# Kernel optimization log

Measured on AMD Instinct MI355X. Metric: run time of the kernel, lower is better.

Reference implementation:

```python
import jax, jax.numpy as jnp
import numpy as np
from math import ceil

SCALE = (0.25, 0.25)
IM_SIZE = (1080, 1920)
KERNEL_WIDTH = 4.0


def _cubic(x):
    absx = np.abs(x)
    absx2 = absx * absx
    absx3 = absx2 * absx
    return ((1.5 * absx3 - 2.5 * absx2 + 1) * (absx <= 1)
            + (-0.5 * absx3 + 2.5 * absx2 - 4 * absx + 2) * ((1 < absx) * (absx <= 2)))


def _contributions(in_length, out_length, scale):
    # MATLAB-style imresize contributions (matches the torch module's numpy code)
    if scale < 1:
        h = lambda v: scale * _cubic(scale * v)
        kernel_width = KERNEL_WIDTH / scale
    else:
        h = _cubic
        kernel_width = KERNEL_WIDTH
    x = np.arange(1, out_length + 1).astype(np.float64)
    u = x / scale + 0.5 * (1 - 1 / scale)
    left = np.floor(u - kernel_width / 2)
    P = int(ceil(kernel_width)) + 2
    ind = np.expand_dims(left, axis=1) + np.arange(P) - 1
    indices = ind.astype(np.int32)
    weights = h(np.expand_dims(u, axis=1) - indices - 1)
    weights = weights / np.sum(weights, axis=1, keepdims=True)
    aux = np.concatenate((np.arange(in_length), np.arange(in_length - 1, -1, -1))).astype(np.int32)
    indices = aux[np.mod(indices, aux.size)]
    keep = np.nonzero(np.any(weights, axis=0))[0]
    return weights[:, keep].astype(np.float32), indices[:, keep].astype(np.int64)


def setup_inputs() -> dict:
    key = jax.random.key(0)
    B, C = 8, 3
    H, W = IM_SIZE
    x = jax.random.normal(key, (B, C, H, W), dtype=jnp.float32)
    out_h = int(ceil(SCALE[0] * H))
    out_w = int(ceil(SCALE[1] * W))
    w_h, idx_h = _contributions(H, out_h, SCALE[0])
    w_w, idx_w = _contributions(W, out_w, SCALE[1])
    return {
        "x": x,
        "w_h": jnp.asarray(w_h), "idx_h": jnp.asarray(idx_h),
        "w_w": jnp.asarray(w_w), "idx_w": jnp.asarray(idx_w),
    }


def reference(x, w_h, idx_h, w_w, idx_w):
    # x: [B, C, H, W] -> work in [B, H, W, C] like the torch transpose dance
    xb = jnp.transpose(x, (0, 2, 3, 1))
    # scale is equal along both axes -> argsort order is [0, 1]: resize H then W
    # gather rows: [B, outH, P, W, C], contract over P with weights [outH, P]
    g = xb[:, idx_h, :, :]
    xb = jnp.einsum("op,bopwc->bowc", w_h, g)
    # gather cols: [B, outH, outW, P, C]
    g = xb[:, :, idx_w, :]
    xb = jnp.einsum("op,bhopc->bhoc", w_w, g)
    return jnp.transpose(xb, (0, 3, 1, 2))
```

## Files before the change

kernel.cpp:

```cpp
#include <hip/hip_runtime.h>

namespace {

constexpr int H  = 1080;
constexpr int W  = 1920;
constexpr int OH = 270;
constexpr int OW = 480;
constexpr int KT = 16;
constexpr int G  = 7;
constexpr int NCHUNK = 38;
constexpr int COLS = 1024;
constexpr int VSTRIDE = 1028;

__global__ __launch_bounds__(256) void bicubic_tile(
    const float* __restrict__ x,
    const float* __restrict__ wh,
    const float* __restrict__ ww,
    float*       __restrict__ out)
{
    __shared__ float vbuf[G * VSTRIDE];

    const int tid  = threadIdx.x;
    const int tile = blockIdx.x;
    const int oh0  = 2 + G * blockIdx.y;
    const int bc   = blockIdx.z;

    const int ow_base = (tile == 0) ? 2   : 255;
    const int Nw      = (tile == 0) ? 253 : 223;
    const int c0      = 4 * ow_base - 6;
    const int r0      = 4 * oh0 - 6;

    float wr[KT];
    __builtin_memcpy(wr, wh + (size_t)oh0 * KT, sizeof(wr));

    int c = c0 + 4 * tid;
    if (c > W - 4) c = W - 4;
    const float* __restrict__ col = x + ((size_t)bc * H + (size_t)r0) * W + c;

    float acc[4][4];
    #pragma unroll
    for (int m = 0; m < 4; ++m)
        #pragma unroll
        for (int cc = 0; cc < 4; ++cc) acc[m][cc] = 0.0f;

    for (int q = 0; q < G + 3; ++q) {
        #pragma unroll
        for (int p = 0; p < 4; ++p) {
            float v[4];
            __builtin_memcpy(v, col + (size_t)(4 * q + p) * W, 16);
            #pragma unroll
            for (int cc = 0; cc < 4; ++cc) {
                acc[0][cc] = fmaf(wr[p],      v[cc], acc[0][cc]);
                acc[1][cc] = fmaf(wr[4 + p],  v[cc], acc[1][cc]);
                acc[2][cc] = fmaf(wr[8 + p],  v[cc], acc[2][cc]);
                acc[3][cc] = fmaf(wr[12 + p], v[cc], acc[3][cc]);
            }
        }
        if (q >= 3) {
            __builtin_memcpy(&vbuf[(q - 3) * VSTRIDE + 4 * tid], acc[3], 16);
        }
        #pragma unroll
        for (int cc = 0; cc < 4; ++cc) {
            acc[3][cc] = acc[2][cc];
            acc[2][cc] = acc[1][cc];
            acc[1][cc] = acc[0][cc];
            acc[0][cc] = 0.0f;
        }
    }
    __syncthreads();

    if (tid < Nw) {
        const int ow = ow_base + tid;
        float wt[KT];
        __builtin_memcpy(wt, ww + (size_t)ow * KT, sizeof(wt));
        float* __restrict__ obase =
            out + ((size_t)bc * OH + oh0) * OW + ow;
        #pragma unroll
        for (int t = 0; t < G; ++t) {
            float v[KT];
            __builtin_memcpy(v, &vbuf[t * VSTRIDE + 4 * tid], sizeof(v));
            float s0 = 0.f, s1 = 0.f;
            #pragma unroll
            for (int k = 0; k < KT; k += 2) {
                s0 = fmaf(v[k],     wt[k],     s0);
                s1 = fmaf(v[k + 1], wt[k + 1], s1);
            }
            obase[(size_t)t * OW] = s0 + s1;
        }
    }
}

constexpr int EDGE_FULL = 4 * OW;
constexpr int EDGE_TOT  = EDGE_FULL + (OH - 4) * 4;

__global__ __launch_bounds__(256) void bicubic_edge(
    const float* __restrict__ x,
    const float* __restrict__ wh,
    const int*   __restrict__ ih,
    const float* __restrict__ ww,
    const int*   __restrict__ iw,
    float*       __restrict__ out)
{
    const int idx = blockIdx.x * blockDim.x + threadIdx.x;
    const int bc  = blockIdx.y;
    if (idx >= EDGE_TOT) return;

    int oh, ow;
    if (idx < EDGE_FULL) {
        int e = idx / OW;
        ow = idx - e * OW;
        oh = (e < 2) ? e : OH - 4 + e;
    } else {
        int t = idx - EDGE_FULL;
        int e = t & 3;
        oh = 2 + (t >> 2);
        ow = (e < 2) ? e : OW - 4 + e;
    }

    const float* __restrict__ img = x + (size_t)bc * ((size_t)H * W);

    float wt[KT];
    __builtin_memcpy(wt, ww + (size_t)ow * KT, sizeof(wt));
    int ir[KT];
    __builtin_memcpy(ir, iw + (size_t)ow * KT, sizeof(ir));

    bool fast = true;
    #pragma unroll
    for (int k = 1; k < KT; ++k) fast = fast && (ir[k] == ir[0] + k);
    const int i0 = ir[0];

    float acc = 0.0f;
    #pragma unroll 4
    for (int kh = 0; kh < KT; ++kh) {
        const int   r = ih[oh * KT + kh];
        const float w = wh[oh * KT + kh];
        const float* row = img + (size_t)r * W;
        float h = 0.0f;
        if (fast) {
            float v[KT];
            __builtin_memcpy(v, row + i0, sizeof(v));
            #pragma unroll
            for (int k = 0; k < KT; ++k) h = fmaf(v[k], wt[k], h);
        } else {
            #pragma unroll
            for (int k = 0; k < KT; ++k) h = fmaf(row[ir[k]], wt[k], h);
        }
        acc = fmaf(w, h, acc);
    }
    out[((size_t)bc * OH + oh) * OW + ow] = acc;
}

__global__ __launch_bounds__(256) void bicubic_generic(
    const float* __restrict__ x,
    const float* __restrict__ wh,
    const int*   __restrict__ ih,
    const float* __restrict__ ww,
    const int*   __restrict__ iw,
    float*       __restrict__ out,
    int Kh, int Kw, int total)
{
    int t = blockIdx.x * blockDim.x + threadIdx.x;
    if (t >= total) return;
    int ow = t % OW;
    int oh = (t / OW) % OH;
    int bc = t / (OW * OH);
    const float* img = x + (size_t)bc * ((size_t)H * W);
    float acc = 0.0f;
    for (int kh = 0; kh < Kh; ++kh) {
        const int   r = ih[oh * Kh + kh];
        const float w = wh[oh * Kh + kh];
        const float* row = img + (size_t)r * W;
        float h = 0.0f;
        for (int k = 0; k < Kw; ++k)
            h = fmaf(row[iw[ow * Kw + k]], ww[ow * Kw + k], h);
        acc = fmaf(w, h, acc);
    }
    out[t] = acc;
}

}

extern "C" void kernel_launch(void* const* d_in, const int* in_sizes, int n_in,
                              void* d_out, int out_size, void* d_ws, size_t ws_size,
                              hipStream_t stream) {
    const float* x  = (const float*)d_in[0];
    const float* wh = (const float*)d_in[1];
    const int*   ih = (const int*)d_in[2];
    const float* ww = (const float*)d_in[3];
    const int*   iw = (const int*)d_in[4];
    float*       out = (float*)d_out;

    const int BC = in_sizes[0] / (H * W);
    const int Kh = in_sizes[1] / OH;
    const int Kw = in_sizes[3] / OW;

    if (Kh == KT && Kw == KT) {
        dim3 mg(2, NCHUNK, BC);
        bicubic_tile<<<mg, 256, 0, stream>>>(x, wh, ww, out);
        dim3 eg((EDGE_TOT + 255) / 256, BC, 1);
        bicubic_edge<<<eg, 256, 0, stream>>>(x, wh, ih, ww, iw, out);
    } else {
        int total = BC * OH * OW;
        bicubic_generic<<<(total + 255) / 256, 256, 0, stream>>>(
            x, wh, ih, ww, iw, out, Kh, Kw, total);
    }
}
```

Before: 325.4 us.

## Fuse edge and tile kernels into one launch with register double-buffered row loads

Merges the interior tile kernel and the border kernel into a single launch, with extra grid rows doing the edge outputs, so one kernel launch and its tail are removed. The interior row loop now prefetches the next four rows into registers while the current ones are being accumulated, and is kept rolled. Column tile bases are shifted so that global loads start 16-byte aligned, with matching offsets into the shared buffer. In exchange the register count per thread goes up, and edge blocks share the kernel's shared-memory allocation, which may lower occupancy.

Result: slower. 337.7 us (+3.8%).

```diff
diff --git a/kernel.cpp b/kernel.cpp
--- a/kernel.cpp
+++ b/kernel.cpp
@@ -9,91 +9,13 @@
 constexpr int KT = 16;
 constexpr int G  = 7;
 constexpr int NCHUNK = 38;
-constexpr int COLS = 1024;
 constexpr int VSTRIDE = 1028;
-
-__global__ __launch_bounds__(256) void bicubic_tile(
-    const float* __restrict__ x,
-    const float* __restrict__ wh,
-    const float* __restrict__ ww,
-    float*       __restrict__ out)
-{
-    __shared__ float vbuf[G * VSTRIDE];
-
-    const int tid  = threadIdx.x;
-    const int tile = blockIdx.x;
-    const int oh0  = 2 + G * blockIdx.y;
-    const int bc   = blockIdx.z;
-
-    const int ow_base = (tile == 0) ? 2   : 255;
-    const int Nw      = (tile == 0) ? 253 : 223;
-    const int c0      = 4 * ow_base - 6;
-    const int r0      = 4 * oh0 - 6;
-
-    float wr[KT];
-    __builtin_memcpy(wr, wh + (size_t)oh0 * KT, sizeof(wr));
-
-    int c = c0 + 4 * tid;
-    if (c > W - 4) c = W - 4;
-    const float* __restrict__ col = x + ((size_t)bc * H + (size_t)r0) * W + c;
-
-    float acc[4][4];
-    #pragma unroll
-    for (int m = 0; m < 4; ++m)
-        #pragma unroll
-        for (int cc = 0; cc < 4; ++cc) acc[m][cc] = 0.0f;
-
-    for (int q = 0; q < G + 3; ++q) {
-        #pragma unroll
-        for (int p = 0; p < 4; ++p) {
-            float v[4];
-            __builtin_memcpy(v, col + (size_t)(4 * q + p) * W, 16);
-            #pragma unroll
-            for (int cc = 0; cc < 4; ++cc) {
-                acc[0][cc] = fmaf(wr[p],      v[cc], acc[0][cc]);
-                acc[1][cc] = fmaf(wr[4 + p],  v[cc], acc[1][cc]);
-                acc[2][cc] = fmaf(wr[8 + p],  v[cc], acc[2][cc]);
-                acc[3][cc] = fmaf(wr[12 + p], v[cc], acc[3][cc]);
-            }
-        }
-        if (q >= 3) {
-            __builtin_memcpy(&vbuf[(q - 3) * VSTRIDE + 4 * tid], acc[3], 16);
-        }
-        #pragma unroll
-        for (int cc = 0; cc < 4; ++cc) {
-            acc[3][cc] = acc[2][cc];
-            acc[2][cc] = acc[1][cc];
-            acc[1][cc] = acc[0][cc];
-            acc[0][cc] = 0.0f;
-        }
-    }
-    __syncthreads();
-
-    if (tid < Nw) {
-        const int ow = ow_base + tid;
-        float wt[KT];
-        __builtin_memcpy(wt, ww + (size_t)ow * KT, sizeof(wt));
-        float* __restrict__ obase =
-            out + ((size_t)bc * OH + oh0) * OW + ow;
-        #pragma unroll
-        for (int t = 0; t < G; ++t) {
-            float v[KT];
-            __builtin_memcpy(v, &vbuf[t * VSTRIDE + 4 * tid], sizeof(v));
-            float s0 = 0.f, s1 = 0.f;
-            #pragma unroll
-            for (int k = 0; k < KT; k += 2) {
-                s0 = fmaf(v[k],     wt[k],     s0);
-                s1 = fmaf(v[k + 1], wt[k + 1], s1);
-            }
-            obase[(size_t)t * OW] = s0 + s1;
-        }
-    }
-}
 
 constexpr int EDGE_FULL = 4 * OW;
 constexpr int EDGE_TOT  = EDGE_FULL + (OH - 4) * 4;
-
-__global__ __launch_bounds__(256) void bicubic_edge(
+constexpr int EDGE_YS   = 6;
+
+__global__ __launch_bounds__(256) void bicubic_fused(
     const float* __restrict__ x,
     const float* __restrict__ wh,
     const int*   __restrict__ ih,
@@ -101,53 +23,148 @@
     const int*   __restrict__ iw,
     float*       __restrict__ out)
 {
-    const int idx = blockIdx.x * blockDim.x + threadIdx.x;
-    const int bc  = blockIdx.y;
-    if (idx >= EDGE_TOT) return;
-
-    int oh, ow;
-    if (idx < EDGE_FULL) {
-        int e = idx / OW;
-        ow = idx - e * OW;
-        oh = (e < 2) ? e : OH - 4 + e;
-    } else {
-        int t = idx - EDGE_FULL;
-        int e = t & 3;
-        oh = 2 + (t >> 2);
-        ow = (e < 2) ? e : OW - 4 + e;
-    }
-
-    const float* __restrict__ img = x + (size_t)bc * ((size_t)H * W);
-
-    float wt[KT];
-    __builtin_memcpy(wt, ww + (size_t)ow * KT, sizeof(wt));
-    int ir[KT];
-    __builtin_memcpy(ir, iw + (size_t)ow * KT, sizeof(ir));
-
-    bool fast = true;
+    __shared__ float vbuf[G * VSTRIDE];
+
+    const int tid = threadIdx.x;
+    const int bx  = blockIdx.x;
+    const int by  = blockIdx.y;
+    const int bc  = blockIdx.z;
+
+    if (by >= NCHUNK) {
+        const int e   = (by - NCHUNK) * 2 + bx;
+        const int idx = e * 256 + tid;
+        if (idx >= EDGE_TOT) return;
+
+        int oh, ow;
+        if (idx < EDGE_FULL) {
+            int q = idx / OW;
+            ow = idx - q * OW;
+            oh = (q < 2) ? q : OH - 4 + q;
+        } else {
+            int t = idx - EDGE_FULL;
+            int q = t & 3;
+            oh = 2 + (t >> 2);
+            ow = (q < 2) ? q : OW - 4 + q;
+        }
+
+        const float* __restrict__ img = x + (size_t)bc * ((size_t)H * W);
+
+        float wt[KT];
+        __builtin_memcpy(wt, ww + (size_t)ow * KT, sizeof(wt));
+        int ir[KT];
+        __builtin_memcpy(ir, iw + (size_t)ow * KT, sizeof(ir));
+
+        bool fastc = true;
+        #pragma unroll
+        for (int k = 1; k < KT; ++k) fastc = fastc && (ir[k] == ir[0] + k);
+        const int i0 = ir[0];
+
+        float acc = 0.0f;
+        #pragma unroll 4
+        for (int kh = 0; kh < KT; ++kh) {
+            const int   r = ih[oh * KT + kh];
+            const float w = wh[oh * KT + kh];
+            const float* row = img + (size_t)r * W;
+            float h = 0.0f;
+            if (fastc) {
+                float v[KT];
+                __builtin_memcpy(v, row + i0, sizeof(v));
+                #pragma unroll
+                for (int k = 0; k < KT; ++k) h = fmaf(v[k], wt[k], h);
+            } else {
+                #pragma unroll
+                for (int k = 0; k < KT; ++k) h = fmaf(row[ir[k]], wt[k], h);
+            }
+            acc = fmaf(w, h, acc);
+        }
+        out[((size_t)bc * OH + oh) * OW + ow] = acc;
+        return;
+    }
+
+    const int owb = bx ? 254 : 2;
+    const int Nw  = bx ? 224 : 252;
+    const int c0  = 4 * owb - 8;
+    const int oh0 = 2 + G * by;
+    const int r0  = 4 * oh0 - 6;
+
+    float wr[KT];
+    __builtin_memcpy(wr, wh + (size_t)oh0 * KT, sizeof(wr));
+
+    int c = c0 + 4 * tid;
+    if (c > W - 4) c = W - 4;
+    const float* __restrict__ p =
+        x + ((size_t)bc * H + (size_t)r0) * W + c;
+
+    float acc[4][4];
     #pragma unroll
-    for (int k = 1; k < KT; ++k) fast = fast && (ir[k] == ir[0] + k);
-    const int i0 = ir[0];
-
-    float acc = 0.0f;
-    #pragma unroll 4
-    for (int kh = 0; kh < KT; ++kh) {
-        const int   r = ih[oh * KT + kh];
-        const float w = wh[oh * KT + kh];
-        const float* row = img + (size_t)r * W;
-        float h = 0.0f;
-        if (fast) {
+    for (int m = 0; m < 4; ++m)
+        #pragma unroll
+        for (int cc = 0; cc < 4; ++cc) acc[m][cc] = 0.0f;
+
+    float cur[4][4];
+    #pragma unroll
+    for (int pp = 0; pp < 4; ++pp)
+        __builtin_memcpy(cur[pp], p + (size_t)pp * W, 16);
+    p += (size_t)4 * W;
+
+    #pragma unroll 1
+    for (int q = 0; q < G + 3; ++q) {
+        float nxt[4][4];
+        if (q < G + 2) {
+            #pragma unroll
+            for (int pp = 0; pp < 4; ++pp)
+                __builtin_memcpy(nxt[pp], p + (size_t)pp * W, 16);
+            p += (size_t)4 * W;
+        }
+        #pragma unroll
+        for (int pp = 0; pp < 4; ++pp)
+            #pragma unroll
+            for (int cc = 0; cc < 4; ++cc) {
+                const float v = cur[pp][cc];
+                acc[0][cc] = fmaf(wr[pp],      v, acc[0][cc]);
+                acc[1][cc] = fmaf(wr[4 + pp],  v, acc[1][cc]);
+                acc[2][cc] = fmaf(wr[8 + pp],  v, acc[2][cc]);
+                acc[3][cc] = fmaf(wr[12 + pp], v, acc[3][cc]);
+            }
+        if (q >= 3) {
+            __builtin_memcpy(&vbuf[(q - 3) * VSTRIDE + 4 * tid + 2],
+                             acc[3], 16);
+        }
+        #pragma unroll
+        for (int cc = 0; cc < 4; ++cc) {
+            acc[3][cc] = acc[2][cc];
+            acc[2][cc] = acc[1][cc];
+            acc[1][cc] = acc[0][cc];
+            acc[0][cc] = 0.0f;
+        }
+        if (q < G + 2) {
+            #pragma unroll
+            for (int pp = 0; pp < 4; ++pp)
+                #pragma unroll
+                for (int cc = 0; cc < 4; ++cc) cur[pp][cc] = nxt[pp][cc];
+        }
+    }
+    __syncthreads();
+
+    if (tid < Nw) {
+        const int ow = owb + tid;
+        float wt[KT];
+        __builtin_memcpy(wt, ww + (size_t)ow * KT, sizeof(wt));
+        float* __restrict__ obase =
+            out + ((size_t)bc * OH + oh0) * OW + ow;
+        #pragma unroll
+        for (int t = 0; t < G; ++t) {
             float v[KT];
-            __builtin_memcpy(v, row + i0, sizeof(v));
-            #pragma unroll
-            for (int k = 0; k < KT; ++k) h = fmaf(v[k], wt[k], h);
-        } else {
-            #pragma unroll
-            for (int k = 0; k < KT; ++k) h = fmaf(row[ir[k]], wt[k], h);
-        }
-        acc = fmaf(w, h, acc);
-    }
-    out[((size_t)bc * OH + oh) * OW + ow] = acc;
+            __builtin_memcpy(v, &vbuf[t * VSTRIDE + 4 * tid + 4], sizeof(v));
+            float s0 = 0.f, s1 = 0.f;
+            #pragma unroll
+            for (int k = 0; k < KT; k += 2) {
+                s0 = fmaf(v[k],     wt[k],     s0);
+                s1 = fmaf(v[k + 1], wt[k + 1], s1);
+            }
+            obase[(size_t)t * OW] = s0 + s1;
+        }
+    }
 }
 
 __global__ __launch_bounds__(256) void bicubic_generic(
@@ -195,10 +212,8 @@
     const int Kw = in_sizes[3] / OW;
 
     if (Kh == KT && Kw == KT) {
-        dim3 mg(2, NCHUNK, BC);
-        bicubic_tile<<<mg, 256, 0, stream>>>(x, wh, ww, out);
-        dim3 eg((EDGE_TOT + 255) / 256, BC, 1);
-        bicubic_edge<<<eg, 256, 0, stream>>>(x, wh, ih, ww, iw, out);
+        dim3 grid(2, NCHUNK + EDGE_YS, BC);
+        bicubic_fused<<<grid, 256, 0, stream>>>(x, wh, ih, ww, iw, out);
     } else {
         int total = BC * OH * OW;
         bicubic_generic<<<(total + 255) / 256, 256, 0, stream>>>(
```
